# Kernel tuning notes

Measured on AMD Instinct MI355X. Metric: run time of the kernel, lower is better.

## Reference

```python
import jax, jax.numpy as jnp
import numpy as np

D_MODEL = 512
N_HEADS = 8
DH = D_MODEL // N_HEADS


def _split_heads(x, h):
    B, L, D = x.shape
    return x.reshape(B, L, h, D // h).transpose(0, 2, 1, 3)  # [B,h,L,Dh]


def setup_inputs() -> dict:
    key = jax.random.key(0)
    ks = jax.random.split(key, 10)
    B, La, Lb, Lc = 4, 256, 256, 32
    s = 1.0 / np.sqrt(D_MODEL)
    return {
        "Q_in": jax.random.normal(ks[0], (B, La, D_MODEL), jnp.float32),
        "K_in": jax.random.normal(ks[1], (B, Lb, D_MODEL), jnp.float32),
        "V_in": jax.random.normal(ks[2], (B, Lb, D_MODEL), jnp.float32),
        "C_tokens": jax.random.normal(ks[3], (B, Lc, D_MODEL), jnp.float32),
        "Wq": jax.random.normal(ks[4], (D_MODEL, D_MODEL), jnp.float32) * s,
        "bq": jnp.zeros((D_MODEL,), jnp.float32),
        "Wk": jax.random.normal(ks[5], (D_MODEL, D_MODEL), jnp.float32) * s,
        "bk": jnp.zeros((D_MODEL,), jnp.float32),
        "Wv": jax.random.normal(ks[6], (D_MODEL, D_MODEL), jnp.float32) * s,
        "bv": jnp.zeros((D_MODEL,), jnp.float32),
    }


def reference(Q_in, K_in, V_in, C_tokens, Wq, bq, Wk, bk, Wv, bv):
    B, La, D = Q_in.shape
    Lb = K_in.shape[1]
    Lc = C_tokens.shape[1]
    h = N_HEADS
    # torch Linear: y = x @ W.T + b
    Q = _split_heads(Q_in @ Wq.T + bq, h)        # [B,h,La,Dh]
    K = _split_heads(K_in @ Wk.T + bk, h)        # [B,h,Lb,Dh]
    V = _split_heads(V_in @ Wv.T + bv, h)        # [B,h,Lb,Dh]
    C = _split_heads(C_tokens, h)                # [B,h,Lc,Dh]
    # tri-linear TSDP score: [B,h,La,Lb,Lc]
    scores = jnp.einsum('bhqd,bhkd,bhcd->bhqkc', Q, K, C) / np.sqrt(DH)
    scores = scores.reshape(B, h, La, Lb * Lc)
    attn = jax.nn.softmax(scores, axis=-1)       # no mask path; all_masked trivially False
    attn5 = attn.reshape(B, h, La, Lb, Lc)
    # cv_mode='mul': VC[k,c,d] = V[k,d]*C[c,d]; fuse contraction, never materialize VC
    out = jnp.einsum('bhqkc,bhkd,bhcd->bhqd', attn5, V, C)
    out = out.transpose(0, 2, 1, 3).reshape(B, La, D)
    return (out, attn)
```

## Files before the change

### kernel.cpp

```cpp
#include <hip/hip_runtime.h>
#include <hip/hip_bf16.h>
#include <math.h>

#define D_MODEL 512
#define NH 8
#define DH 64
#define LA 256
#define LB 256
#define LC 32
#define BATCH 4
#define KC_TOT 8192
#define XN (BATCH * LA * D_MODEL)
#define WN (D_MODEL * D_MODEL)

typedef float f32x4 __attribute__((ext_vector_type(4)));
typedef _Float16 f16x8 __attribute__((ext_vector_type(8)));
typedef _Float16 f16x4 __attribute__((ext_vector_type(4)));
typedef unsigned int u32;

#if __has_builtin(__builtin_amdgcn_exp2f)
#define EXP2(x) __builtin_amdgcn_exp2f(x)
#else
#define EXP2(x) exp2f(x)
#endif
#define SCLOG2E 0.18033688011118324f

#define MFMA16F(a, b, c) __builtin_amdgcn_mfma_f32_16x16x32_f16(a, b, c, 0, 0, 0)

static __device__ __forceinline__ u32 pkrtz(float x, float y) {
  auto t = __builtin_amdgcn_cvt_pkrtz(x, y);
  u32 r; __builtin_memcpy(&r, &t, 4);
  return r;
}

__global__ __launch_bounds__(256) void cvt_kernel(
    const float* __restrict__ X0, const float* __restrict__ X1,
    const float* __restrict__ X2, const float* __restrict__ W0,
    const float* __restrict__ W1, const float* __restrict__ W2,
    _Float16* __restrict__ dst)
{
  const int t = blockIdx.y;
  const float* src;
  size_t n, off;
  switch (t) {
    case 0: src = X0; n = XN; off = 0; break;
    case 1: src = X1; n = XN; off = (size_t)XN; break;
    case 2: src = X2; n = XN; off = 2 * (size_t)XN; break;
    case 3: src = W0; n = WN; off = 3 * (size_t)XN; break;
    case 4: src = W1; n = WN; off = 3 * (size_t)XN + WN; break;
    default: src = W2; n = WN; off = 3 * (size_t)XN + 2 * (size_t)WN; break;
  }
  const size_t i = (size_t)blockIdx.x * 2048 + threadIdx.x * 8;
  if (i >= n) return;
  float4 a = *(const float4*)(src + i);
  float4 b = *(const float4*)(src + i + 4);
  f16x8 r;
  r[0] = (_Float16)a.x; r[1] = (_Float16)a.y; r[2] = (_Float16)a.z; r[3] = (_Float16)a.w;
  r[4] = (_Float16)b.x; r[5] = (_Float16)b.y; r[6] = (_Float16)b.z; r[7] = (_Float16)b.w;
  *(f16x8*)(dst + off + i) = r;
}

__global__ __launch_bounds__(256) void proj_mfma(
    const _Float16* __restrict__ XWh,
    const float* __restrict__ bq, const float* __restrict__ bk,
    const float* __restrict__ bv,
    _Float16* __restrict__ Qp, _Float16* __restrict__ Kp,
    _Float16* __restrict__ Vp)
{
  const int z = blockIdx.z;
  const _Float16* X = XWh + (size_t)z * XN;
  const _Float16* W = XWh + 3 * (size_t)XN + (size_t)z * WN;
  const float* bias = (z == 0) ? bq : (z == 1) ? bk : bv;
  _Float16* Y = (z == 0) ? Qp : (z == 1) ? Kp : Vp;

  const int tid = threadIdx.x;
  const int lane = tid & 63;
  const int w = tid >> 6;
  const int l16 = lane & 15;
  const int lg = lane >> 4;

  const int n0 = blockIdx.x * 64;
  const int m0 = blockIdx.y * 64;
  const int m = m0 + w * 16 + l16;

  f32x4 acc[4] = {};
  const _Float16* xrow = X + (size_t)m * D_MODEL;
  const _Float16* wbase = W + (size_t)(n0 + l16) * D_MODEL;

#pragma unroll 4
  for (int ks = 0; ks < 16; ++ks) {
    f16x8 bf = *(const f16x8*)(xrow + ks * 32 + lg * 8);
#pragma unroll
    for (int ai = 0; ai < 4; ++ai) {
      f16x8 af = *(const f16x8*)(wbase + (size_t)(ai * 16) * D_MODEL + ks * 32 + lg * 8);
      acc[ai] = MFMA16F(af, bf, acc[ai]);
    }
  }
#pragma unroll
  for (int ai = 0; ai < 4; ++ai) {
    float4 b4 = *(const float4*)&bias[n0 + ai * 16 + lg * 4];
    f16x4 r;
    r[0] = (_Float16)(acc[ai][0] + b4.x);
    r[1] = (_Float16)(acc[ai][1] + b4.y);
    r[2] = (_Float16)(acc[ai][2] + b4.z);
    r[3] = (_Float16)(acc[ai][3] + b4.w);
    *(f16x4*)&Y[(size_t)m * D_MODEL + n0 + ai * 16 + lg * 4] = r;
  }
}

#define STG 40
__global__ __launch_bounds__(512) void attn_fused(
    const _Float16* __restrict__ Qp, const _Float16* __restrict__ Kp,
    const _Float16* __restrict__ Vp, const float* __restrict__ Ct,
    float* __restrict__ attn, float* __restrict__ out)
{
  __shared__ __align__(16) _Float16 stage[8][2][16][STG];
  __shared__ __align__(16) _Float16 C_lds[LC][DH + 8];
  __shared__ __align__(16) _Float16 CT_lds[DH][LC + 8];
  __shared__ float red_lds[8][16];
  __shared__ float inv_lds[16];

  const int tid = threadIdx.x;
  const int lane = tid & 63;
  const int w = tid >> 6;
  const int l16 = lane & 15;
  const int lg = lane >> 4;

  const int tile = blockIdx.x;
  const int bh = tile >> 4;
  const int qt = tile & 15;
  const int b = bh >> 3;
  const int h = bh & 7;

  const _Float16* Kb = Kp + (size_t)b * LB * D_MODEL + h * DH;
  const _Float16* Vb = Vp + (size_t)b * LB * D_MODEL + h * DH;
  const float* Cb = Ct + (size_t)b * LC * D_MODEL + h * DH;

  for (int i = tid; i < LC * DH; i += 512) {
    const int c = i >> 6, d = i & 63;
    _Float16 v = (_Float16)Cb[(size_t)c * D_MODEL + d];
    C_lds[c][d] = v;
    CT_lds[d][c] = v;
  }

  f16x8 qf[2];
  {
    const _Float16* Qb = Qp + (size_t)(b * LA + qt * 16) * D_MODEL + h * DH;
#pragma unroll
    for (int kh = 0; kh < 2; ++kh)
      qf[kh] = *(const f16x8*)(Qb + (size_t)l16 * D_MODEL + kh * 32 + lg * 8);
  }
  __syncthreads();

  float rs = 0.f;
#pragma unroll 2
  for (int ch = 0; ch < 32; ++ch) {
    const int krow = w * 32 + ch;
    const _Float16* krp = Kb + (size_t)krow * D_MODEL;
    f32x4 s0 = {0.f, 0.f, 0.f, 0.f}, s1 = {0.f, 0.f, 0.f, 0.f};
#pragma unroll
    for (int kh = 0; kh < 2; ++kh) {
      f16x8 kv = *(const f16x8*)(krp + kh * 32 + lg * 8);
      f16x8 c0 = *(const f16x8*)&C_lds[l16][kh * 32 + lg * 8];
      f16x8 c1 = *(const f16x8*)&C_lds[16 + l16][kh * 32 + lg * 8];
      s0 = MFMA16F(kv * c0, qf[kh], s0);
      s1 = MFMA16F(kv * c1, qf[kh], s1);
    }
#pragma unroll
    for (int r = 0; r < 4; ++r)
      rs += EXP2(s0[r] * SCLOG2E) + EXP2(s1[r] * SCLOG2E);
  }
  rs += __shfl_xor(rs, 16);
  rs += __shfl_xor(rs, 32);
  if (lane < 16) red_lds[w][lane] = rs;
  __syncthreads();
  if (tid < 16) {
    float t = 0.f;
#pragma unroll
    for (int ww = 0; ww < 8; ++ww) t += red_lds[ww][tid];
    inv_lds[tid] = 1.f / t;
  }
  __syncthreads();
  const float inv = inv_lds[l16];

  f32x4 oacc[4] = {};
  const int s1i = l16 + ((lg & 1) << 5);
  const int s2i = s1i + 16;
  const int strow = lane >> 3;
  const int stcol = (lane & 7) * 4;
  float* abase = attn + (size_t)(bh * LA + qt * 16) * KC_TOT + w * 1024;

#pragma unroll 2
  for (int ch = 0; ch < 32; ++ch) {
    const int krow = w * 32 + ch;
    const int cur = ch & 1;
    const _Float16* krp = Kb + (size_t)krow * D_MODEL;
    f32x4 s0 = {0.f, 0.f, 0.f, 0.f}, s1 = {0.f, 0.f, 0.f, 0.f};
#pragma unroll
    for (int kh = 0; kh < 2; ++kh) {
      f16x8 kv = *(const f16x8*)(krp + kh * 32 + lg * 8);
      f16x8 c0 = *(const f16x8*)&C_lds[l16][kh * 32 + lg * 8];
      f16x8 c1 = *(const f16x8*)&C_lds[16 + l16][kh * 32 + lg * 8];
      s0 = MFMA16F(kv * c0, qf[kh], s0);
      s1 = MFMA16F(kv * c1, qf[kh], s1);
    }
    f32x4 p0, p1;
#pragma unroll
    for (int r = 0; r < 4; ++r) {
      p0[r] = EXP2(s0[r] * SCLOG2E) * inv;
      p1[r] = EXP2(s1[r] * SCLOG2E) * inv;
    }

    const u32 a0 = pkrtz(p0[0], p0[1]), a1 = pkrtz(p0[2], p0[3]);
    const u32 b0 = pkrtz(p1[0], p1[1]), b1 = pkrtz(p1[2], p1[3]);
    const u32 sa0 = (u32)__shfl((int)a0, s1i), sb0 = (u32)__shfl((int)b0, s1i);
    const u32 sa1 = (u32)__shfl((int)a1, s1i), sb1 = (u32)__shfl((int)b1, s1i);
    const u32 ta0 = (u32)__shfl((int)a0, s2i), tb0 = (u32)__shfl((int)b0, s2i);
    const u32 ta1 = (u32)__shfl((int)a1, s2i), tb1 = (u32)__shfl((int)b1, s2i);
    u32 bw[4];
    bw[0] = (lg < 2) ? sa0 : sb0;
    bw[1] = (lg < 2) ? sa1 : sb1;
    bw[2] = (lg < 2) ? ta0 : tb0;
    bw[3] = (lg < 2) ? ta1 : tb1;
    f16x8 bf; __builtin_memcpy(&bf, bw, 16);

    *(f16x8*)&stage[w][cur][l16][lg * 8] = bf;

    const _Float16* vrow = Vb + (size_t)krow * D_MODEL;
#pragma unroll
    for (int dt = 0; dt < 4; ++dt) {
      const _Float16 vv = vrow[dt * 16 + l16];
      f16x8 ct8 = *(const f16x8*)&CT_lds[dt * 16 + l16][lg * 8];
      oacc[dt] = MFMA16F(ct8 * vv, bf, oacc[dt]);
    }

    if (ch > 0) {
      const int pc = ch - 1;
      const int pb = pc & 1;
      f16x4 h0 = *(const f16x4*)&stage[w][pb][strow][stcol];
      f16x4 h1 = *(const f16x4*)&stage[w][pb][strow + 8][stcol];
      f32x4 v0, v1;
#pragma unroll
      for (int r = 0; r < 4; ++r) { v0[r] = (float)h0[r]; v1[r] = (float)h1[r]; }
      *(f32x4*)(abase + (size_t)strow * KC_TOT + pc * 32 + stcol) = v0;
      *(f32x4*)(abase + (size_t)(strow + 8) * KC_TOT + pc * 32 + stcol) = v1;
    }
  }
  {
    f16x4 h0 = *(const f16x4*)&stage[w][1][strow][stcol];
    f16x4 h1 = *(const f16x4*)&stage[w][1][strow + 8][stcol];
    f32x4 v0, v1;
#pragma unroll
    for (int r = 0; r < 4; ++r) { v0[r] = (float)h0[r]; v1[r] = (float)h1[r]; }
    *(f32x4*)(abase + (size_t)strow * KC_TOT + 31 * 32 + stcol) = v0;
    *(f32x4*)(abase + (size_t)(strow + 8) * KC_TOT + 31 * 32 + stcol) = v1;
  }

  float* obuf = (float*)&stage[0][0][0][0];
  const int idx = l16 * 64 + lane;
  (void)idx;
  __syncthreads();
  if (w >= 4) {
#pragma unroll
    for (int dt = 0; dt < 4; ++dt)
#pragma unroll
      for (int r = 0; r < 4; ++r)
        obuf[(w - 4) * 1024 + l16 * 64 + dt * 16 + lg * 4 + r] = oacc[dt][r];
  }
  __syncthreads();
  if (w < 4) {
#pragma unroll
    for (int dt = 0; dt < 4; ++dt)
#pragma unroll
      for (int r = 0; r < 4; ++r)
        oacc[dt][r] += obuf[w * 1024 + l16 * 64 + dt * 16 + lg * 4 + r];
  }
  __syncthreads();
  if (w >= 2 && w < 4) {
#pragma unroll
    for (int dt = 0; dt < 4; ++dt)
#pragma unroll
      for (int r = 0; r < 4; ++r)
        obuf[(w - 2) * 1024 + l16 * 64 + dt * 16 + lg * 4 + r] = oacc[dt][r];
  }
  __syncthreads();
  if (w < 2) {
#pragma unroll
    for (int dt = 0; dt < 4; ++dt)
#pragma unroll
      for (int r = 0; r < 4; ++r)
        oacc[dt][r] += obuf[w * 1024 + l16 * 64 + dt * 16 + lg * 4 + r];
  }
  __syncthreads();
  if (w == 1) {
#pragma unroll
    for (int dt = 0; dt < 4; ++dt)
#pragma unroll
      for (int r = 0; r < 4; ++r)
        obuf[l16 * 64 + dt * 16 + lg * 4 + r] = oacc[dt][r];
  }
  __syncthreads();
  if (w == 0) {
    const size_t obase = (size_t)(b * LA + qt * 16 + l16) * D_MODEL + h * DH;
#pragma unroll
    for (int dt = 0; dt < 4; ++dt) {
      f32x4 v;
#pragma unroll
      for (int r = 0; r < 4; ++r)
        v[r] = oacc[dt][r] + obuf[l16 * 64 + dt * 16 + lg * 4 + r];
      *(f32x4*)&out[obase + dt * 16 + lg * 4] = v;
    }
  }
}

extern "C" void kernel_launch(void* const* d_in, const int* in_sizes, int n_in,
                              void* d_out, int out_size, void* d_ws, size_t ws_size,
                              hipStream_t stream) {
  const float* Q_in     = (const float*)d_in[0];
  const float* K_in     = (const float*)d_in[1];
  const float* V_in     = (const float*)d_in[2];
  const float* C_tokens = (const float*)d_in[3];
  const float* Wq       = (const float*)d_in[4];
  const float* bq       = (const float*)d_in[5];
  const float* Wk       = (const float*)d_in[6];
  const float* bk       = (const float*)d_in[7];
  const float* Wv       = (const float*)d_in[8];
  const float* bv       = (const float*)d_in[9];

  float* outp  = (float*)d_out;
  float* attnp = outp + (size_t)BATCH * LA * D_MODEL;

  _Float16* Qp  = (_Float16*)d_ws;
  _Float16* Kp  = Qp + (size_t)XN;
  _Float16* Vp  = Kp + (size_t)XN;
  _Float16* XWh = Vp + (size_t)XN;

  cvt_kernel<<<dim3(256, 6), 256, 0, stream>>>(Q_in, K_in, V_in, Wq, Wk, Wv, XWh);
  proj_mfma<<<dim3(8, 16, 3), 256, 0, stream>>>(XWh, bq, bk, bv, Qp, Kp, Vp);
  attn_fused<<<512, 512, 0, stream>>>(Qp, Kp, Vp, C_tokens, attnp, outp);
}
```

Before: 92.45 us.

## Interleave key rows across warps and stage attn tile for row-contiguous writes

Key rows are now interleaved across the eight warps (krow = ch*8 + w), so in each iteration the block as a whole covers 256 contiguous attention columns. All warps publish their probability fragments into one shared double-buffered tile, then after a block-wide barrier each warp writes two full 1 KB row segments of attn. Previously each warp wrote scattered 128 B segments. The aim is wider, more sequential global stores for the large attn output. The cost is a __syncthreads every iteration and the loop unrolling being turned off.

```diff
diff --git a/kernel.cpp b/kernel.cpp
--- a/kernel.cpp
+++ b/kernel.cpp
@@ -108,13 +108,13 @@
   }
 }
 
-#define STG 40
+#define STG 264
 __global__ __launch_bounds__(512) void attn_fused(
     const _Float16* __restrict__ Qp, const _Float16* __restrict__ Kp,
     const _Float16* __restrict__ Vp, const float* __restrict__ Ct,
     float* __restrict__ attn, float* __restrict__ out)
 {
-  __shared__ __align__(16) _Float16 stage[8][2][16][STG];
+  __shared__ __align__(16) _Float16 pub[2][16][STG];
   __shared__ __align__(16) _Float16 C_lds[LC][DH + 8];
   __shared__ __align__(16) _Float16 CT_lds[DH][LC + 8];
   __shared__ float red_lds[8][16];
@@ -155,7 +155,7 @@
   float rs = 0.f;
 #pragma unroll 2
   for (int ch = 0; ch < 32; ++ch) {
-    const int krow = w * 32 + ch;
+    const int krow = ch * 8 + w;
     const _Float16* krp = Kb + (size_t)krow * D_MODEL;
     f32x4 s0 = {0.f, 0.f, 0.f, 0.f}, s1 = {0.f, 0.f, 0.f, 0.f};
 #pragma unroll
@@ -186,13 +186,12 @@
   f32x4 oacc[4] = {};
   const int s1i = l16 + ((lg & 1) << 5);
   const int s2i = s1i + 16;
-  const int strow = lane >> 3;
-  const int stcol = (lane & 7) * 4;
-  float* abase = attn + (size_t)(bh * LA + qt * 16) * KC_TOT + w * 1024;
-
-#pragma unroll 2
+  float* atile = attn + (size_t)(bh * LA + qt * 16) * KC_TOT;
+  const int r0 = 2 * w, r1 = 2 * w + 1;
+
+#pragma unroll 1
   for (int ch = 0; ch < 32; ++ch) {
-    const int krow = w * 32 + ch;
+    const int krow = ch * 8 + w;
     const int cur = ch & 1;
     const _Float16* krp = Kb + (size_t)krow * D_MODEL;
     f32x4 s0 = {0.f, 0.f, 0.f, 0.f}, s1 = {0.f, 0.f, 0.f, 0.f};
@@ -224,7 +223,7 @@
     bw[3] = (lg < 2) ? ta1 : tb1;
     f16x8 bf; __builtin_memcpy(&bf, bw, 16);
 
-    *(f16x8*)&stage[w][cur][l16][lg * 8] = bf;
+    *(f16x8*)&pub[cur][l16][w * 32 + lg * 8] = bf;
 
     const _Float16* vrow = Vb + (size_t)krow * D_MODEL;
 #pragma unroll
@@ -234,31 +233,20 @@
       oacc[dt] = MFMA16F(ct8 * vv, bf, oacc[dt]);
     }
 
-    if (ch > 0) {
-      const int pc = ch - 1;
-      const int pb = pc & 1;
-      f16x4 h0 = *(const f16x4*)&stage[w][pb][strow][stcol];
-      f16x4 h1 = *(const f16x4*)&stage[w][pb][strow + 8][stcol];
+    __syncthreads();
+
+    {
+      f16x4 h0 = *(const f16x4*)&pub[cur][r0][lane * 4];
+      f16x4 h1 = *(const f16x4*)&pub[cur][r1][lane * 4];
       f32x4 v0, v1;
 #pragma unroll
       for (int r = 0; r < 4; ++r) { v0[r] = (float)h0[r]; v1[r] = (float)h1[r]; }
-      *(f32x4*)(abase + (size_t)strow * KC_TOT + pc * 32 + stcol) = v0;
-      *(f32x4*)(abase + (size_t)(strow + 8) * KC_TOT + pc * 32 + stcol) = v1;
-    }
-  }
-  {
-    f16x4 h0 = *(const f16x4*)&stage[w][1][strow][stcol];
-    f16x4 h1 = *(const f16x4*)&stage[w][1][strow + 8][stcol];
-    f32x4 v0, v1;
-#pragma unroll
-    for (int r = 0; r < 4; ++r) { v0[r] = (float)h0[r]; v1[r] = (float)h1[r]; }
-    *(f32x4*)(abase + (size_t)strow * KC_TOT + 31 * 32 + stcol) = v0;
-    *(f32x4*)(abase + (size_t)(strow + 8) * KC_TOT + 31 * 32 + stcol) = v1;
-  }
-
-  float* obuf = (float*)&stage[0][0][0][0];
-  const int idx = l16 * 64 + lane;
-  (void)idx;
+      *(f32x4*)(atile + (size_t)r0 * KC_TOT + ch * 256 + lane * 4) = v0;
+      *(f32x4*)(atile + (size_t)r1 * KC_TOT + ch * 256 + lane * 4) = v1;
+    }
+  }
+
+  float* obuf = (float*)&pub[0][0][0];
   __syncthreads();
   if (w >= 4) {
 #pragma unroll
```

After: 107.9 us. +16.7%, slower.
